# Kernel tuning notes

Hardware: AMD Instinct MI355X
Metric: run time of the kernel (lower is better)

## Reference

```python
import jax, jax.numpy as jnp
import numpy as np

K = 7            # kernel_size (odd, neighborhood width)
H = 16           # num_heads
DIM = 512        # model dim
D = DIM // H     # head_dim = 32
SCALE = D ** (-0.5)


def setup_inputs() -> dict:
    key = jax.random.key(0)
    k0, k1, k2, k3 = jax.random.split(key, 4)
    B, L, C = 2, 16384, DIM
    x = jax.random.normal(k0, (B, L, C), jnp.float32)
    qkv_w = jax.random.normal(k1, (3 * C, C), jnp.float32) * 0.02   # torch Linear weight [out, in]
    qkv_b = jnp.zeros((3 * C,), jnp.float32)
    rpb = jax.random.normal(k2, (H, 2 * K - 1), jnp.float32) * 0.02  # relative positional bias table
    proj_w = jax.random.normal(k3, (C, C), jnp.float32) * 0.02
    proj_b = jnp.zeros((C,), jnp.float32)
    return {"x": x, "qkv_w": qkv_w, "qkv_b": qkv_b, "rpb": rpb,
            "proj_w": proj_w, "proj_b": proj_b}


def reference(x, qkv_w, qkv_b, rpb, proj_w, proj_b):
    B, L, C = x.shape
    # qkv projection: [B, L, 3C] -> [3, B, H, L, D]
    qkv = (x @ qkv_w.T + qkv_b).reshape(B, L, 3, H, D).transpose(2, 0, 3, 1, 4)
    q = qkv[0] * SCALE
    k = qkv[1]
    v = qkv[2]

    # Neighborhood window start per query (clamped at boundaries, NATTEN semantics)
    pos = jnp.arange(L)
    ni = jnp.clip(pos - K // 2, 0, L - K)            # [L]
    idx = ni[:, None] + jnp.arange(K)                 # [L, K] key indices per query

    kg = k[:, :, idx]                                 # [B, H, L, K, D] gathered keys
    vg = v[:, :, idx]                                 # [B, H, L, K, D] gathered values

    # relative positional bias: rpb index = (j - i) + (K - 1)
    bias = rpb[:, idx - pos[:, None] + (K - 1)]       # [H, L, K]

    attn = jnp.einsum('bhld,bhlkd->bhlk', q, kg) + bias[None]
    attn = jax.nn.softmax(attn, axis=-1)              # softmax over the K-neighborhood
    out = jnp.einsum('bhlk,bhlkd->bhld', attn, vg)
    out = out.transpose(0, 2, 1, 3).reshape(B, L, C)
    return out @ proj_w.T + proj_b
```

## Files before the change

### kernel.cpp

```cpp
#include <hip/hip_runtime.h>

typedef unsigned short u16;
typedef unsigned int   u32;
typedef __attribute__((ext_vector_type(8))) short bf16x8;
typedef __attribute__((ext_vector_type(4))) float f32x4;

#define L_SEQ 16384
#define NHEAD 16
#define CDIM  512
#define SCALE 0.17677669529663689f

__device__ __forceinline__ float bf2f(u16 v) {
    union { u32 u; float f; } x; x.u = ((u32)v) << 16; return x.f;
}
__device__ __forceinline__ u16 f2bf(float f) {
    union { u32 u; float f; } x; x.f = f;
    u32 r = x.u + 0x7fff + ((x.u >> 16) & 1);
    return (u16)(r >> 16);
}

__global__ void detect_dtype_kernel(const u16* __restrict__ x, int* __restrict__ flag) {
    __shared__ int cnt;
    if (threadIdx.x == 0) cnt = 0;
    __syncthreads();
    int c = 0;
    for (int k = 0; k < 32; k++) {
        u16 v = x[2 * (threadIdx.x + 256 * k)];
        if ((v & 0x7F80) == 0x7F80) c++;
    }
    atomicAdd(&cnt, c);
    __syncthreads();
    if (threadIdx.x == 0) *flag = (cnt > 0) ? 1 : 0;
}

__global__ __launch_bounds__(256)
void convert_weights_kernel(const void* __restrict__ qkv_w, const void* __restrict__ proj_w,
                            const void* __restrict__ qkv_b, const void* __restrict__ proj_b,
                            const void* __restrict__ rpb, u16* __restrict__ dst,
                            const int* __restrict__ flag) {
    const int f = *flag;
    for (int i = blockIdx.x * 256 + threadIdx.x; i < 1050832; i += gridDim.x * 256) {
        const void* src; int off;
        if (i < 786432)       { src = qkv_w;  off = i; }
        else if (i < 1048576) { src = proj_w; off = i - 786432; }
        else if (i < 1050112) { src = qkv_b;  off = i - 1048576; }
        else if (i < 1050624) { src = proj_b; off = i - 1050112; }
        else                  { src = rpb;    off = i - 1050624; }
        dst[i] = f ? f2bf(((const float*)src)[off]) : ((const u16*)src)[off];
    }
}

__global__ __launch_bounds__(256)
void convert_x_kernel(const void* __restrict__ src, u16* __restrict__ dst,
                      int base_c, int lch, const int* __restrict__ flag) {
    const int f  = *flag;
    const int i0 = (blockIdx.x * 256 + threadIdx.x) * 8;
    const int r  = i0 >> 9;
    const int b  = (r >= lch) ? 1 : 0;
    const size_t s = (size_t)(b * L_SEQ + base_c + (r - b * lch)) * 512 + (i0 & 511);
    if (f) {
        const float* sf = (const float*)src + s;
        union { u16 o[8]; uint4 v; } pk;
        #pragma unroll
        for (int j = 0; j < 8; j++) pk.o[j] = f2bf(sf[j]);
        *(uint4*)(dst + i0) = pk.v;
    } else {
        *(uint4*)(dst + i0) = *(const uint4*)((const u16*)src + s);
    }
}

#define GEMM_CORE(A_PTR, W_PTR, KD, AROW0, N0)                                             \
    __shared__ u16 As[128 * 64];                                                           \
    __shared__ u16 Ws[128 * 64];                                                           \
    const int tid  = threadIdx.x;                                                          \
    const int wave = tid >> 6;                                                             \
    const int lane = tid & 63;                                                             \
    const int quad = lane >> 4;                                                            \
    const int r16  = lane & 15;                                                            \
    const int wm   = (wave >> 1) << 6;                                                     \
    const int wn   = (wave & 1) << 6;                                                      \
    f32x4 acc[4][4];                                                                       \
    _Pragma("unroll")                                                                      \
    for (int i = 0; i < 4; i++)                                                            \
        _Pragma("unroll")                                                                  \
        for (int j = 0; j < 4; j++) acc[i][j] = (f32x4){0.f, 0.f, 0.f, 0.f};               \
    const int lr8 = lane >> 3;                                                             \
    const int swc = ((lane & 7) ^ lr8) << 3;                \
    const u16* ga = (A_PTR) + (size_t)((AROW0) + wave * 8 + lr8) * (KD) + swc;             \
    const u16* gw = (W_PTR) + (size_t)((N0) + wave * 8 + lr8) * (KD) + swc;                \
    u16* asb = As + wave * 512;                                      \
    u16* wsb = Ws + wave * 512;                                                            \
    for (int kt = 0; kt < (KD); kt += 64) {                                                \
        _Pragma("unroll")                                                                  \
        for (int t = 0; t < 4; t++) {                                                      \
            __builtin_amdgcn_global_load_lds(                                              \
                (const __attribute__((address_space(1))) void*)(ga + kt + (size_t)(t * 32) * (KD)), \
                (__attribute__((address_space(3))) void*)(asb + t * 2048), 16, 0, 0);      \
            __builtin_amdgcn_global_load_lds(                                              \
                (const __attribute__((address_space(1))) void*)(gw + kt + (size_t)(t * 32) * (KD)), \
                (__attribute__((address_space(3))) void*)(wsb + t * 2048), 16, 0, 0);      \
        }                                                                                  \
        __syncthreads();                                                                   \
        _Pragma("unroll")                                                                  \
        for (int ks = 0; ks < 2; ks++) {                                                   \
            bf16x8 af[4], bfr[4];                                                          \
            _Pragma("unroll")                                                              \
            for (int mi = 0; mi < 4; mi++)                                                 \
                af[mi] = *(const bf16x8*)&As[(wm + mi * 16 + r16) * 64 +                   \
                                             (((ks * 4 + quad) ^ (r16 & 7)) << 3)];        \
            _Pragma("unroll")                                                              \
            for (int ni = 0; ni < 4; ni++)                                                 \
                bfr[ni] = *(const bf16x8*)&Ws[(wn + ni * 16 + r16) * 64 +                  \
                                              (((ks * 4 + quad) ^ (r16 & 7)) << 3)];       \
            _Pragma("unroll")                                                              \
            for (int mi = 0; mi < 4; mi++)                                                 \
                _Pragma("unroll")                                                          \
                for (int ni = 0; ni < 4; ni++)                                             \
                    acc[mi][ni] = __builtin_amdgcn_mfma_f32_16x16x32_bf16(                 \
                        af[mi], bfr[ni], acc[mi][ni], 0, 0, 0);                            \
        }                                                                                  \
        __syncthreads();                                                                   \
    }

__global__ __launch_bounds__(256)
void gemm_qkv_kernel(const u16* __restrict__ A, const u16* __restrict__ W,
                     const u16* __restrict__ bias, u16* __restrict__ qkv_out, int lch)
{
    const int m0l = blockIdx.x << 7;
    const int n0  = blockIdx.y << 7;
    const int b   = blockIdx.z;
    const size_t plane = (size_t)1024 * lch;
    GEMM_CORE(A, W, 512, b * lch + m0l, n0)
    #pragma unroll
    for (int ni = 0; ni < 4; ni++) {
        const int col   = n0 + wn + ni * 16 + r16;
        const int which = col >> 9;
        const int rem   = col & 511;
        const int h     = rem >> 5;
        const int d     = rem & 31;
        const float bv  = bf2f(bias[col]);
        const float scl = (which == 0) ? SCALE : 1.0f;
        u16* outb = qkv_out + (size_t)which * plane;
        #pragma unroll
        for (int mi = 0; mi < 4; mi++) {
            #pragma unroll
            for (int r = 0; r < 4; r++) {
                const int rrel = m0l + wm + mi * 16 + quad * 4 + r;
                outb[((size_t)(b * NHEAD + h) * lch + rrel) * 32 + d] =
                    f2bf((acc[mi][ni][r] + bv) * scl);
            }
        }
    }
}

__global__ __launch_bounds__(256)
void attn_kernel(const uint4* __restrict__ q, const uint4* __restrict__ k,
                 const uint4* __restrict__ v, const u16* __restrict__ rpb,
                 uint4* __restrict__ outa, int c0, int base_c, int lc_shift, int lch)
{
    const int grp = blockIdx.x * 64 + (threadIdx.x >> 2);
    const int d4  = threadIdx.x & 3;
    const int lr  = grp & ((1 << lc_shift) - 1);
    const int bh  = grp >> lc_shift;
    const int h   = bh & 15;
    const int l   = c0 + lr;
    const size_t base = (size_t)bh * lch * 4;

    const uint4 qp = q[base + (size_t)(l - base_c) * 4 + d4];
    float qf[8];
    qf[0] = bf2f((u16)qp.x); qf[1] = bf2f((u16)(qp.x >> 16));
    qf[2] = bf2f((u16)qp.y); qf[3] = bf2f((u16)(qp.y >> 16));
    qf[4] = bf2f((u16)qp.z); qf[5] = bf2f((u16)(qp.z >> 16));
    qf[6] = bf2f((u16)qp.w); qf[7] = bf2f((u16)(qp.w >> 16));

    int ni = l - 3;
    if (ni < 0) ni = 0;
    if (ni > L_SEQ - 7) ni = L_SEQ - 7;
    const int rn = ni - base_c;

    float logit[7];
    #pragma unroll
    for (int j = 0; j < 7; j++) {
        const uint4 kp = k[base + (size_t)(rn + j) * 4 + d4];
        float p;
        p  = qf[0] * bf2f((u16)kp.x) + qf[1] * bf2f((u16)(kp.x >> 16));
        p += qf[2] * bf2f((u16)kp.y) + qf[3] * bf2f((u16)(kp.y >> 16));
        p += qf[4] * bf2f((u16)kp.z) + qf[5] * bf2f((u16)(kp.z >> 16));
        p += qf[6] * bf2f((u16)kp.w) + qf[7] * bf2f((u16)(kp.w >> 16));
        p += __shfl_xor(p, 1, 64);
        p += __shfl_xor(p, 2, 64);
        logit[j] = p + bf2f(rpb[h * 13 + (ni + j - l + 6)]);
    }
    float mx = logit[0];
    #pragma unroll
    for (int j = 1; j < 7; j++) mx = fmaxf(mx, logit[j]);
    float s = 0.f, w[7];
    #pragma unroll
    for (int j = 0; j < 7; j++) { w[j] = __expf(logit[j] - mx); s += w[j]; }
    const float inv = 1.0f / s;
    float o[8] = {0.f, 0.f, 0.f, 0.f, 0.f, 0.f, 0.f, 0.f};
    #pragma unroll
    for (int j = 0; j < 7; j++) {
        const uint4 vp = v[base + (size_t)(rn + j) * 4 + d4];
        o[0] += w[j] * bf2f((u16)vp.x); o[1] += w[j] * bf2f((u16)(vp.x >> 16));
        o[2] += w[j] * bf2f((u16)vp.y); o[3] += w[j] * bf2f((u16)(vp.y >> 16));
        o[4] += w[j] * bf2f((u16)vp.z); o[5] += w[j] * bf2f((u16)(vp.z >> 16));
        o[6] += w[j] * bf2f((u16)vp.w); o[7] += w[j] * bf2f((u16)(vp.w >> 16));
    }
    uint4 pk;
    pk.x = (u32)f2bf(o[0] * inv) | ((u32)f2bf(o[1] * inv) << 16);
    pk.y = (u32)f2bf(o[2] * inv) | ((u32)f2bf(o[3] * inv) << 16);
    pk.z = (u32)f2bf(o[4] * inv) | ((u32)f2bf(o[5] * inv) << 16);
    pk.w = (u32)f2bf(o[6] * inv) | ((u32)f2bf(o[7] * inv) << 16);
    outa[((size_t)(((bh >> 4) << lc_shift) + lr)) * 64 + h * 4 + d4] = pk;
}

__global__ __launch_bounds__(256)
void gemm_proj_kernel(const u16* __restrict__ A, const u16* __restrict__ W,
                      const u16* __restrict__ bias, void* __restrict__ out,
                      int c0, int lc, const int* __restrict__ flag)
{
    const int m0l = blockIdx.x << 7;
    const int n0  = blockIdx.y << 7;
    const int b   = blockIdx.z;
    GEMM_CORE(A, W, 512, b * lc + m0l, n0)
    const int f = *flag;
    #pragma unroll
    for (int ni = 0; ni < 4; ni++) {
        const int col  = n0 + wn + ni * 16 + r16;
        const float bv = bf2f(bias[col]);
        #pragma unroll
        for (int mi = 0; mi < 4; mi++) {
            #pragma unroll
            for (int r = 0; r < 4; r++) {
                const int lr = m0l + wm + mi * 16 + quad * 4 + r;
                const size_t idx = (size_t)(b * L_SEQ + c0 + lr) * CDIM + col;
                const float val = acc[mi][ni][r] + bv;
                if (f) ((float*)out)[idx] = val;
                else   ((u16*)out)[idx]   = f2bf(val);
            }
        }
    }
}

extern "C" void kernel_launch(void* const* d_in, const int* in_sizes, int n_in,
                              void* d_out, int out_size, void* d_ws, size_t ws_size,
                              hipStream_t stream) {
    const void* x      = d_in[0];
    const void* qkv_w  = d_in[1];
    const void* qkv_b  = d_in[2];
    const void* rpb    = d_in[3];
    const void* proj_w = d_in[4];
    const void* proj_b = d_in[5];

    int nchunk, lch, lc, lc_shift;
    static const int c0sA[1] = {0},                 basesA[1] = {0};
    static const int c0sB[2] = {0, 8192},           basesB[2] = {0, 8064};
    static const int c0sC[8] = {0, 2048, 4096, 6144, 8192, 10240, 12288, 14336};
    static const int basesC[8] = {0, 1984, 4032, 6080, 8128, 10176, 12224, 14208};
    const int* c0s; const int* bases;
    if (ws_size >= (size_t)2 * (16 + 1050880 + (size_t)4096 * 16384 + 1024 * 16384)) {
        nchunk = 1; lch = 16384; lc = 16384; lc_shift = 14; c0s = c0sA; bases = basesA;
    } else if (ws_size >= (size_t)2 * (16 + 1050880 + (size_t)4096 * 8320 + 1024 * 8192)) {
        nchunk = 2; lch = 8320;  lc = 8192;  lc_shift = 13; c0s = c0sB; bases = basesB;
    } else {
        nchunk = 8; lch = 2176;  lc = 2048;  lc_shift = 11; c0s = c0sC; bases = basesC;
    }

    u16* ws    = (u16*)d_ws;
    int* flag  = (int*)ws;
    u16* wseg  = ws + 16;
    u16* wqkv  = wseg;
    u16* wproj = wseg + 786432;
    u16* bqkv  = wseg + 1048576;
    u16* bproj = wseg + 1050112;
    u16* rpbc  = wseg + 1050624;
    u16* xc    = ws + 16 + 1050880;
    u16* qkv   = xc + (size_t)1024 * lch;
    u16* wsa   = qkv + (size_t)3072 * lch;

    detect_dtype_kernel<<<1, 256, 0, stream>>>((const u16*)x, flag);
    convert_weights_kernel<<<2048, 256, 0, stream>>>(qkv_w, proj_w, qkv_b, proj_b,
                                                     rpb, wseg, flag);

    for (int c = 0; c < nchunk; c++) {
        convert_x_kernel<<<lch / 2, 256, 0, stream>>>(x, xc, bases[c], lch, flag);
        gemm_qkv_kernel<<<dim3(lch / 128, 12, 2), 256, 0, stream>>>(
            xc, wqkv, bqkv, qkv, lch);
        attn_kernel<<<lc / 2, 256, 0, stream>>>(
            (const uint4*)qkv, (const uint4*)(qkv + (size_t)1024 * lch),
            (const uint4*)(qkv + (size_t)2048 * lch), rpbc,
            (uint4*)wsa, c0s[c], bases[c], lc_shift, lch);
        gemm_proj_kernel<<<dim3(lc / 128, 4, 2), 256, 0, stream>>>(
            wsa, wproj, bproj, d_out, c0s[c], lc, flag);
    }
}
```

Baseline: 295.5 us.

## Replace GEMM core with 256x256 tile, double-buffered LDS pipeline and 8 waves

Swaps the 128x128 single-buffered GEMM core used by the QKV and projection GEMMs for a 256x256 tile run by 512 threads. The new core double-buffers LDS, issues the next k-slice's global-to-LDS loads while MFMAs run, and uses explicit vmcnt waits, barriers and setprio. The goal is to hide global load latency and raise data reuse per tile. In exchange it uses 64KB of LDS and more accumulator registers per block, so fewer blocks fit per CU and grids are smaller. The chunk halo sizes are changed to keep lch a multiple of 256.

```diff
diff --git a/kernel.cpp b/kernel.cpp
--- a/kernel.cpp
+++ b/kernel.cpp
@@ -69,85 +69,110 @@
     }
 }
 
-#define GEMM_CORE(A_PTR, W_PTR, KD, AROW0, N0)                                             \
-    __shared__ u16 As[128 * 64];                                                           \
-    __shared__ u16 Ws[128 * 64];                                                           \
-    const int tid  = threadIdx.x;                                                          \
-    const int wave = tid >> 6;                                                             \
-    const int lane = tid & 63;                                                             \
-    const int quad = lane >> 4;                                                            \
-    const int r16  = lane & 15;                                                            \
-    const int wm   = (wave >> 1) << 6;                                                     \
-    const int wn   = (wave & 1) << 6;                                                      \
-    f32x4 acc[4][4];                                                                       \
-    _Pragma("unroll")                                                                      \
-    for (int i = 0; i < 4; i++)                                                            \
-        _Pragma("unroll")                                                                  \
-        for (int j = 0; j < 4; j++) acc[i][j] = (f32x4){0.f, 0.f, 0.f, 0.f};               \
-    const int lr8 = lane >> 3;                                                             \
-    const int swc = ((lane & 7) ^ lr8) << 3;                \
-    const u16* ga = (A_PTR) + (size_t)((AROW0) + wave * 8 + lr8) * (KD) + swc;             \
-    const u16* gw = (W_PTR) + (size_t)((N0) + wave * 8 + lr8) * (KD) + swc;                \
-    u16* asb = As + wave * 512;                                      \
-    u16* wsb = Ws + wave * 512;                                                            \
-    for (int kt = 0; kt < (KD); kt += 64) {                                                \
-        _Pragma("unroll")                                                                  \
-        for (int t = 0; t < 4; t++) {                                                      \
-            __builtin_amdgcn_global_load_lds(                                              \
-                (const __attribute__((address_space(1))) void*)(ga + kt + (size_t)(t * 32) * (KD)), \
-                (__attribute__((address_space(3))) void*)(asb + t * 2048), 16, 0, 0);      \
-            __builtin_amdgcn_global_load_lds(                                              \
-                (const __attribute__((address_space(1))) void*)(gw + kt + (size_t)(t * 32) * (KD)), \
-                (__attribute__((address_space(3))) void*)(wsb + t * 2048), 16, 0, 0);      \
-        }                                                                                  \
-        __syncthreads();                                                                   \
-        _Pragma("unroll")                                                                  \
-        for (int ks = 0; ks < 2; ks++) {                                                   \
-            bf16x8 af[4], bfr[4];                                                          \
-            _Pragma("unroll")                                                              \
-            for (int mi = 0; mi < 4; mi++)                                                 \
-                af[mi] = *(const bf16x8*)&As[(wm + mi * 16 + r16) * 64 +                   \
-                                             (((ks * 4 + quad) ^ (r16 & 7)) << 3)];        \
-            _Pragma("unroll")                                                              \
-            for (int ni = 0; ni < 4; ni++)                                                 \
-                bfr[ni] = *(const bf16x8*)&Ws[(wn + ni * 16 + r16) * 64 +                  \
-                                              (((ks * 4 + quad) ^ (r16 & 7)) << 3)];       \
-            _Pragma("unroll")                                                              \
-            for (int mi = 0; mi < 4; mi++)                                                 \
-                _Pragma("unroll")                                                          \
-                for (int ni = 0; ni < 4; ni++)                                             \
-                    acc[mi][ni] = __builtin_amdgcn_mfma_f32_16x16x32_bf16(                 \
-                        af[mi], bfr[ni], acc[mi][ni], 0, 0, 0);                            \
-        }                                                                                  \
-        __syncthreads();                                                                   \
-    }
-
-__global__ __launch_bounds__(256)
+#define VM4   asm volatile("s_waitcnt vmcnt(4)" ::: "memory")
+#define VM0   asm volatile("s_waitcnt vmcnt(0)" ::: "memory")
+#define LGKM0 asm volatile("s_waitcnt lgkmcnt(0)" ::: "memory")
+#define NOOP  ((void)0)
+
+#define PHASE(P, KS, CH, STAGE_STMT, WAIT_STMT)                                         \
+    {                                                                                   \
+        if ((CH) == 0) {                                                                \
+            _Pragma("unroll")                                                           \
+            for (int i_ = 0; i_ < 4; i_++)                                              \
+                bb[i_] = *(const bf16x8*)&lds[P][1][KS][boff + i_ * 512];               \
+        }                                                                               \
+        _Pragma("unroll")                                                               \
+        for (int i_ = 0; i_ < 4; i_++)                                                  \
+            af[i_] = *(const bf16x8*)&lds[P][0][KS][aoff + ((CH) * 4 + i_) * 512];      \
+        STAGE_STMT;                                                                     \
+        WAIT_STMT;                                                                      \
+        __builtin_amdgcn_s_barrier();                                                   \
+        LGKM0;                                                                          \
+        __builtin_amdgcn_s_setprio(1);                                                  \
+        _Pragma("unroll")                                                               \
+        for (int mi_ = 0; mi_ < 4; mi_++)                                               \
+            _Pragma("unroll")                                                           \
+            for (int ni_ = 0; ni_ < 4; ni_++)                                           \
+                acc[(CH) * 4 + mi_][ni_] = __builtin_amdgcn_mfma_f32_16x16x32_bf16(     \
+                    af[mi_], bb[ni_], acc[(CH) * 4 + mi_][ni_], 0, 0, 0);               \
+        __builtin_amdgcn_s_setprio(0);                                                  \
+        __builtin_amdgcn_s_barrier();                                                   \
+    }
+
+#define GEMM256_CORE(A_PTR, W_PTR, AROW0, N0)                                           \
+    __shared__ u16 lds[2][2][2][8192];            \
+    const int tid  = threadIdx.x;                                                       \
+    const int wave = tid >> 6;                                                          \
+    const int lane = tid & 63;                                                          \
+    const int quad = lane >> 4;                                                         \
+    const int r16  = lane & 15;                                                         \
+    const int wm2  = wave >> 2;                                                         \
+    const int wn4  = wave & 3;                                                          \
+    f32x4 acc[8][4];                                                                    \
+    _Pragma("unroll")                                                                   \
+    for (int i = 0; i < 8; i++)                                                         \
+        _Pragma("unroll")                                                               \
+        for (int j = 0; j < 4; j++) acc[i][j] = (f32x4){0.f, 0.f, 0.f, 0.f};            \
+    const int lr4  = lane >> 2;                                                         \
+    const int swc2 = (((lane & 3) ^ ((lane >> 3) & 3)) << 3);                           \
+    const u16* gA = (A_PTR) + (size_t)((AROW0) + wave * 16 + lr4) * 512 + swc2;         \
+    const u16* gW = (W_PTR) + (size_t)((N0)    + wave * 16 + lr4) * 512 + swc2;         \
+    const int rsw  = (quad ^ ((r16 >> 1) & 3)) << 3;                                    \
+    const int aoff = (wm2 * 128 + r16) * 32 + rsw;                                      \
+    const int boff = (wn4 * 64  + r16) * 32 + rsw;                                      \
+    const int sdst = wave * 512;                                 \
+    bf16x8 af[4], bb[4];                                                                \
+    auto STAGE = [&](int P2, int OP, int KT, int KS) {                                  \
+        const u16* g = (OP ? gW : gA) + KT * 64 + KS * 32;                              \
+        u16* d0 = &lds[P2][OP][KS][sdst];                                               \
+        __builtin_amdgcn_global_load_lds(                                               \
+            (const __attribute__((address_space(1))) void*)g,                           \
+            (__attribute__((address_space(3))) void*)d0, 16, 0, 0);                     \
+        __builtin_amdgcn_global_load_lds(                                               \
+            (const __attribute__((address_space(1))) void*)(g + (size_t)128 * 512),     \
+            (__attribute__((address_space(3))) void*)(d0 + 4096), 16, 0, 0);            \
+    };                                                                                  \
+    STAGE(0, 0, 0, 0); STAGE(0, 1, 0, 0); STAGE(0, 0, 0, 1); STAGE(0, 1, 0, 1);         \
+    VM4;                                                                                \
+    __builtin_amdgcn_s_barrier();                                                       \
+    for (int T = 0; T < 7; T++) {                                                       \
+        const int p = T & 1, pn = p ^ 1;                                                \
+        PHASE(p, 0, 0, STAGE(pn, 0, T + 1, 0), NOOP);                                   \
+        PHASE(p, 0, 1, STAGE(pn, 1, T + 1, 0), VM4);                                    \
+        PHASE(p, 1, 0, STAGE(pn, 0, T + 1, 1), NOOP);                                   \
+        PHASE(p, 1, 1, STAGE(pn, 1, T + 1, 1), VM4);                                    \
+    }                                                                                   \
+    PHASE(1, 0, 0, NOOP, NOOP);                                                         \
+    PHASE(1, 0, 1, NOOP, VM0);                                                          \
+    PHASE(1, 1, 0, NOOP, NOOP);                                                         \
+    PHASE(1, 1, 1, NOOP, NOOP);
+
+__global__ __launch_bounds__(512, 2)
 void gemm_qkv_kernel(const u16* __restrict__ A, const u16* __restrict__ W,
                      const u16* __restrict__ bias, u16* __restrict__ qkv_out, int lch)
 {
-    const int m0l = blockIdx.x << 7;
-    const int n0  = blockIdx.y << 7;
+    const int m0l = blockIdx.x << 8;
+    const int n0  = blockIdx.y << 8;
     const int b   = blockIdx.z;
     const size_t plane = (size_t)1024 * lch;
-    GEMM_CORE(A, W, 512, b * lch + m0l, n0)
+    GEMM256_CORE(A, W, b * lch + m0l, n0)
     #pragma unroll
     for (int ni = 0; ni < 4; ni++) {
-        const int col   = n0 + wn + ni * 16 + r16;
+        const int col   = n0 + wn4 * 64 + ni * 16 + r16;
         const int which = col >> 9;
         const int rem   = col & 511;
         const int h     = rem >> 5;
         const int d     = rem & 31;
         const float bv  = bf2f(bias[col]);
         const float scl = (which == 0) ? SCALE : 1.0f;
-        u16* outb = qkv_out + (size_t)which * plane;
+        u16* outb = qkv_out + (size_t)which * plane +
+                    ((size_t)(b * NHEAD + h) * lch) * 32 + d;
         #pragma unroll
-        for (int mi = 0; mi < 4; mi++) {
+        for (int mi = 0; mi < 8; mi++) {
             #pragma unroll
             for (int r = 0; r < 4; r++) {
-                const int rrel = m0l + wm + mi * 16 + quad * 4 + r;
-                outb[((size_t)(b * NHEAD + h) * lch + rrel) * 32 + d] =
-                    f2bf((acc[mi][ni][r] + bv) * scl);
+                const int rrel = m0l + wm2 * 128 + mi * 16 + quad * 4 + r;
+                outb[(size_t)rrel * 32] = f2bf((acc[mi][ni][r] + bv) * scl);
             }
         }
     }
@@ -215,25 +240,25 @@
     outa[((size_t)(((bh >> 4) << lc_shift) + lr)) * 64 + h * 4 + d4] = pk;
 }
 
-__global__ __launch_bounds__(256)
+__global__ __launch_bounds__(512, 2)
 void gemm_proj_kernel(const u16* __restrict__ A, const u16* __restrict__ W,
                       const u16* __restrict__ bias, void* __restrict__ out,
                       int c0, int lc, const int* __restrict__ flag)
 {
-    const int m0l = blockIdx.x << 7;
-    const int n0  = blockIdx.y << 7;
+    const int m0l = blockIdx.x << 8;
+    const int n0  = blockIdx.y << 8;
     const int b   = blockIdx.z;
-    GEMM_CORE(A, W, 512, b * lc + m0l, n0)
+    GEMM256_CORE(A, W, b * lc + m0l, n0)
     const int f = *flag;
     #pragma unroll
     for (int ni = 0; ni < 4; ni++) {
-        const int col  = n0 + wn + ni * 16 + r16;
+        const int col  = n0 + wn4 * 64 + ni * 16 + r16;
         const float bv = bf2f(bias[col]);
         #pragma unroll
-        for (int mi = 0; mi < 4; mi++) {
+        for (int mi = 0; mi < 8; mi++) {
             #pragma unroll
             for (int r = 0; r < 4; r++) {
-                const int lr = m0l + wm + mi * 16 + quad * 4 + r;
+                const int lr = m0l + wm2 * 128 + mi * 16 + quad * 4 + r;
                 const size_t idx = (size_t)(b * L_SEQ + c0 + lr) * CDIM + col;
                 const float val = acc[mi][ni][r] + bv;
                 if (f) ((float*)out)[idx] = val;
@@ -255,16 +280,16 @@
 
     int nchunk, lch, lc, lc_shift;
     static const int c0sA[1] = {0},                 basesA[1] = {0};
-    static const int c0sB[2] = {0, 8192},           basesB[2] = {0, 8064};
+    static const int c0sB[2] = {0, 8192},           basesB[2] = {0, 7936};
     static const int c0sC[8] = {0, 2048, 4096, 6144, 8192, 10240, 12288, 14336};
-    static const int basesC[8] = {0, 1984, 4032, 6080, 8128, 10176, 12224, 14208};
+    static const int basesC[8] = {0, 1920, 3968, 6016, 8064, 10112, 12160, 14080};
     const int* c0s; const int* bases;
     if (ws_size >= (size_t)2 * (16 + 1050880 + (size_t)4096 * 16384 + 1024 * 16384)) {
         nchunk = 1; lch = 16384; lc = 16384; lc_shift = 14; c0s = c0sA; bases = basesA;
-    } else if (ws_size >= (size_t)2 * (16 + 1050880 + (size_t)4096 * 8320 + 1024 * 8192)) {
-        nchunk = 2; lch = 8320;  lc = 8192;  lc_shift = 13; c0s = c0sB; bases = basesB;
+    } else if (ws_size >= (size_t)2 * (16 + 1050880 + (size_t)4096 * 8448 + 1024 * 8192)) {
+        nchunk = 2; lch = 8448;  lc = 8192;  lc_shift = 13; c0s = c0sB; bases = basesB;
     } else {
-        nchunk = 8; lch = 2176;  lc = 2048;  lc_shift = 11; c0s = c0sC; bases = basesC;
+        nchunk = 8; lch = 2304;  lc = 2048;  lc_shift = 11; c0s = c0sC; bases = basesC;
     }
 
     u16* ws    = (u16*)d_ws;
@@ -285,13 +310,13 @@
 
     for (int c = 0; c < nchunk; c++) {
         convert_x_kernel<<<lch / 2, 256, 0, stream>>>(x, xc, bases[c], lch, flag);
-        gemm_qkv_kernel<<<dim3(lch / 128, 12, 2), 256, 0, stream>>>(
+        gemm_qkv_kernel<<<dim3(lch / 256, 6, 2), 512, 0, stream>>>(
             xc, wqkv, bqkv, qkv, lch);
         attn_kernel<<<lc / 2, 256, 0, stream>>>(
             (const uint4*)qkv, (const uint4*)(qkv + (size_t)1024 * lch),
             (const uint4*)(qkv + (size_t)2048 * lch), rpbc,
             (uint4*)wsa, c0s[c], bases[c], lc_shift, lch);
-        gemm_proj_kernel<<<dim3(lc / 128, 4, 2), 256, 0, stream>>>(
+        gemm_proj_kernel<<<dim3(lc / 256, 2, 2), 512, 0, stream>>>(
             wsa, wproj, bproj, d_out, c0s[c], lc, flag);
     }
 }
```

Result: faster. 281.0 us (-4.9%).
